# Kernel optimization log

Measured on AMD Instinct MI355X. Metric: run time of the kernel, lower is better.

## Reference

```python
import jax, jax.numpy as jnp
import numpy as np

FUZZYNUM = 4
EPS = 1e-5  # torch BatchNorm2d default


def conv2d(x, w, b):
    y = jax.lax.conv_general_dilated(x, w, (1, 1), 'SAME',
                                     dimension_numbers=('NCHW', 'OIHW', 'NCHW'))
    return y + b[None, :, None, None]


def batchnorm(x, gamma, beta):
    # training-mode BN: batch statistics over (N,H,W), biased variance
    m = jnp.mean(x, axis=(0, 2, 3), keepdims=True)
    v = jnp.mean((x - m) ** 2, axis=(0, 2, 3), keepdims=True)
    xn = (x - m) * jax.lax.rsqrt(v + EPS)
    return xn * gamma[None, :, None, None] + beta[None, :, None, None]


def fuzzify(x, lb_all, ub_all):
    # x: (N,1,H,W) -- conv1 output has 1 channel, so only bounds[0, f] are used.
    # Per-f sequential semantics of the original loop (x is mutated across f):
    #  in-range (ld>0 & ud>0): add exp(-0.5 ld^2)+exp(-0.5 ud^2)
    #  out-of-range (ld<0 or ud<0): reflect x -> 2*lb - x, then add
    #      exp(-0.5 ld^2) + exp(-0.5 (ub - x_new)^2)
    #  (the other sub-branches in the source are mathematically unreachable)
    fuzz = jnp.zeros_like(x)
    for f in range(FUZZYNUM):
        lb = lb_all[0, f]
        ub = ub_all[0, f]
        ld = x - lb
        ud = ub - x
        in_range = (ld > 0) & (ud > 0)
        out_range = (ld < 0) | (ud < 0)
        x_ref = 2.0 * lb - x
        c_in = jnp.exp(-0.5 * ld ** 2) + jnp.exp(-0.5 * ud ** 2)
        c_out = jnp.exp(-0.5 * ld ** 2) + jnp.exp(-0.5 * (ub - x_ref) ** 2)
        fuzz = fuzz + jnp.where(in_range, c_in, jnp.where(out_range, c_out, 0.0))
        x = jnp.where(out_range, x_ref, x)
    return fuzz


def setup_inputs() -> dict:
    key = jax.random.key(0)
    k0, k1, k2 = jax.random.split(key, 3)
    N, C, H, W = 16, 64, 256, 256
    sigma, init_mean = 2.0, 0.2
    x = jax.random.normal(k0, (N, C, H, W), dtype=jnp.float32)
    bnd1 = 1.0 / np.sqrt(C * 9)
    bnd2 = 1.0 / np.sqrt(1 * 9)
    conv1_w = jax.random.uniform(k1, (1, C, 3, 3), jnp.float32, -bnd1, bnd1)
    conv2_w = jax.random.uniform(k2, (C, 1, 3, 3), jnp.float32, -bnd2, bnd2)
    center = jnp.full((C, FUZZYNUM), init_mean, jnp.float32)
    return {
        'x': x,
        'conv1_w': conv1_w,
        'conv1_b': jnp.zeros((1,), jnp.float32),
        'conv2_w': conv2_w,
        'conv2_b': jnp.zeros((C,), jnp.float32),
        'bn1_g': jnp.ones((1,), jnp.float32),
        'bn1_b': jnp.zeros((1,), jnp.float32),
        'bn2_g': jnp.ones((C,), jnp.float32),
        'bn2_b': jnp.zeros((C,), jnp.float32),
        'lower_bound': center - sigma,
        'upper_bound': center + sigma,
    }


def reference(x, conv1_w, conv1_b, conv2_w, conv2_b, bn1_g, bn1_b, bn2_g, bn2_b,
              lower_bound, upper_bound):
    h = batchnorm(conv2d(x, conv1_w, conv1_b), bn1_g, bn1_b)  # (N,1,H,W)
    fz = fuzzify(h, lower_bound, upper_bound)                  # (N,1,H,W)
    return batchnorm(conv2d(fz, conv2_w, conv2_b), bn2_g, bn2_b)  # (N,C,H,W)
```

## Files before the change

### kernel.cpp

```cpp
#include <hip/hip_runtime.h>
#include <cstdint>

#define EPS 1e-5f
#define INV_NTOT (1.0f / 1048576.0f)

#define FZ_OFF  1048576
#define ST_OFF  2097152

__device__ __forceinline__ void dev_atomic_add(float* p, float v) {
    __hip_atomic_fetch_add(p, v, __ATOMIC_RELAXED, __HIP_MEMORY_SCOPE_AGENT);
}

__global__ __launch_bounds__(512) void k1_conv1(
    const float* __restrict__ x, const float* __restrict__ w1,
    float* __restrict__ h0, float* __restrict__ stats)
{
    __shared__ float tile[10][264];
    __shared__ float red_s[8], red_q[8];

    const int tid   = threadIdx.x;
    const int bid   = blockIdx.x;
    const int n     = bid >> 5;
    const int ht    = bid & 31;
    const int h0b   = ht << 3;

    const int t     = tid & 255;
    const int ohb   = (tid >> 8) << 2;
    const int rs    = tid >> 6;
    const int col4  = (tid & 63) << 2;

    float acc0 = 0.f, acc1 = 0.f, acc2 = 0.f, acc3 = 0.f;

    if (tid < 10) { tile[tid][3] = 0.f; tile[tid][260] = 0.f; }

    const float* xn = x + ((size_t)n << 22);

    for (int c = 0; c < 64; ++c) {
        __syncthreads();
        {
            int g = h0b - 1 + rs;
            float4 v = make_float4(0.f, 0.f, 0.f, 0.f);
            if ((unsigned)g < 256u)
                v = *(const float4*)(xn + ((size_t)c << 16) + (g << 8) + col4);
            *(float4*)&tile[rs][4 + col4] = v;
            if (rs < 2) {
                int g2 = h0b + 7 + rs;
                float4 v2 = make_float4(0.f, 0.f, 0.f, 0.f);
                if ((unsigned)g2 < 256u)
                    v2 = *(const float4*)(xn + ((size_t)c << 16) + (g2 << 8) + col4);
                *(float4*)&tile[8 + rs][4 + col4] = v2;
            }
        }
        __syncthreads();

        float wc[9];
        #pragma unroll
        for (int k = 0; k < 9; ++k) wc[k] = w1[c * 9 + k];

        #pragma unroll
        for (int rr = 0; rr < 6; ++rr) {
            const int sr = ohb + rr;
            float vm = tile[sr][3 + t];
            float v0 = tile[sr][4 + t];
            float vp = tile[sr][5 + t];
            #pragma unroll
            for (int di = 0; di < 3; ++di) {
                const int l = rr - di;
                if (l >= 0 && l < 4) {
                    float contrib = wc[di * 3 + 0] * vm + wc[di * 3 + 1] * v0
                                  + wc[di * 3 + 2] * vp;
                    if      (l == 0) acc0 += contrib;
                    else if (l == 1) acc1 += contrib;
                    else if (l == 2) acc2 += contrib;
                    else             acc3 += contrib;
                }
            }
        }
    }

    size_t ob = ((size_t)n << 16) + (size_t)((h0b + ohb) << 8) + t;
    h0[ob]       = acc0;
    h0[ob + 256] = acc1;
    h0[ob + 512] = acc2;
    h0[ob + 768] = acc3;

    float s  = acc0 + acc1 + acc2 + acc3;
    float sq = acc0 * acc0 + acc1 * acc1 + acc2 * acc2 + acc3 * acc3;
    #pragma unroll
    for (int o = 32; o > 0; o >>= 1) {
        s  += __shfl_down(s,  o, 64);
        sq += __shfl_down(sq, o, 64);
    }
    const int wave = tid >> 6, lane = tid & 63;
    if (lane == 0) { red_s[wave] = s; red_q[wave] = sq; }
    __syncthreads();
    if (tid == 0) {
        float S = 0.f, Q = 0.f;
        #pragma unroll
        for (int i = 0; i < 8; ++i) { S += red_s[i]; Q += red_q[i]; }
        dev_atomic_add(&stats[0], S);
        dev_atomic_add(&stats[1], Q);
    }
}

__global__ __launch_bounds__(256) void k3_fuzzify(
    const float* __restrict__ h0, const float* __restrict__ stats,
    const float* __restrict__ bn1_g, const float* __restrict__ bn1_b,
    const float* __restrict__ lb, const float* __restrict__ ub,
    float* __restrict__ fz)
{
    const int i = blockIdx.x * 256 + threadIdx.x;

    const float mean = stats[0] * INV_NTOT;
    const float var  = stats[1] * INV_NTOT - mean * mean;
    const float rstd = rsqrtf(var + EPS);
    const float A    = bn1_g[0] * rstd;
    const float B    = bn1_b[0] - mean * A;

    float lbv[4], ubv[4];
    #pragma unroll
    for (int f = 0; f < 4; ++f) { lbv[f] = lb[f]; ubv[f] = ub[f]; }

    float4 hv = *(const float4*)(h0 + (size_t)i * 4);
    float in[4] = { hv.x, hv.y, hv.z, hv.w };
    float res[4];
    #pragma unroll
    for (int k = 0; k < 4; ++k) {
        float xv = A * in[k] + B;
        float fuzz = 0.f;
        #pragma unroll
        for (int f = 0; f < 4; ++f) {
            float ld = xv - lbv[f];
            float ud = ubv[f] - xv;
            bool inr  = (ld > 0.f) && (ud > 0.f);
            bool outr = (ld < 0.f) || (ud < 0.f);
            float xr  = 2.f * lbv[f] - xv;
            float u2  = ubv[f] - xr;
            float e1  = __expf(-0.5f * ld * ld);
            float cin  = e1 + __expf(-0.5f * ud * ud);
            float cout = e1 + __expf(-0.5f * u2 * u2);
            fuzz += inr ? cin : (outr ? cout : 0.f);
            xv = outr ? xr : xv;
        }
        res[k] = fuzz;
    }
    *(float4*)(fz + (size_t)i * 4) = make_float4(res[0], res[1], res[2], res[3]);
}

__global__ __launch_bounds__(256) void k4_stats(
    const float* __restrict__ fz, float* __restrict__ stats)
{
    float s9[9], q45[45];
    #pragma unroll
    for (int i = 0; i < 9; ++i)  s9[i]  = 0.f;
    #pragma unroll
    for (int i = 0; i < 45; ++i) q45[i] = 0.f;

    const int base = blockIdx.x * 256 + threadIdx.x;
    for (int k = 0; k < 16; ++k) {
        int p = base + k * 65536;
        int w = p & 255, h = (p >> 8) & 255, n = p >> 16;
        const float* f = fz + ((size_t)n << 16);
        float v[9];
        #pragma unroll
        for (int di = 0; di < 3; ++di)
            #pragma unroll
            for (int dj = 0; dj < 3; ++dj) {
                int hh = h + di - 1, ww = w + dj - 1;
                v[di * 3 + dj] = ((unsigned)hh < 256u && (unsigned)ww < 256u)
                               ? f[(hh << 8) + ww] : 0.f;
            }
        int idx = 0;
        #pragma unroll
        for (int a = 0; a < 9; ++a) {
            s9[a] += v[a];
            #pragma unroll
            for (int b = a; b < 9; ++b) q45[idx++] += v[a] * v[b];
        }
    }

    __shared__ float red[4][54];
    const int wave = threadIdx.x >> 6, lane = threadIdx.x & 63;
    float vals[54];
    #pragma unroll
    for (int i = 0; i < 9; ++i)  vals[i]     = s9[i];
    #pragma unroll
    for (int i = 0; i < 45; ++i) vals[9 + i] = q45[i];
    #pragma unroll
    for (int i = 0; i < 54; ++i) {
        float vv = vals[i];
        #pragma unroll
        for (int o = 32; o > 0; o >>= 1) vv += __shfl_down(vv, o, 64);
        if (lane == 0) red[wave][i] = vv;
    }
    __syncthreads();
    if (threadIdx.x < 54) {
        float tot = red[0][threadIdx.x] + red[1][threadIdx.x]
                  + red[2][threadIdx.x] + red[3][threadIdx.x];
        dev_atomic_add(&stats[2 + threadIdx.x], tot);
    }
}

__global__ void k5_finalize(
    const float* __restrict__ w2, const float* __restrict__ bn2_g,
    const float* __restrict__ bn2_b, float* __restrict__ stats)
{
    const int c = threadIdx.x;
    if (c >= 64) return;
    float w[9];
    #pragma unroll
    for (int k = 0; k < 9; ++k) w[k] = w2[c * 9 + k];
    float P = 0.f;
    #pragma unroll
    for (int k = 0; k < 9; ++k) P += w[k] * stats[2 + k];
    P *= INV_NTOT;
    float QF = 0.f;
    int idx = 0;
    #pragma unroll
    for (int a = 0; a < 9; ++a)
        #pragma unroll
        for (int b = a; b < 9; ++b) {
            float qv = stats[11 + idx]; idx++;
            QF += w[a] * w[b] * qv * ((a == b) ? 1.f : 2.f);
        }
    QF *= INV_NTOT;
    float var   = QF - P * P;
    float scale = bn2_g[c] * rsqrtf(var + EPS);
    float bias  = bn2_b[c] - P * scale;
    stats[56 + c]  = scale;
    stats[120 + c] = bias;
}

__global__ __launch_bounds__(256) void k6_conv2(
    const float* __restrict__ fz, const float* __restrict__ w2,
    const float* __restrict__ stats, float* __restrict__ out)
{
    __shared__ float tile[34][36];
    const int bid = blockIdx.x;
    const int n   = bid >> 6;
    const int th  = (bid >> 3) & 7;
    const int tw  = bid & 7;
    const int h0b = th << 5, w0b = tw << 5;
    const int tid = threadIdx.x;

    const float* f = fz + ((size_t)n << 16);
    for (int i = tid; i < 34 * 34; i += 256) {
        int rr = i / 34, cc = i - rr * 34;
        int gh = h0b + rr - 1, gw = w0b + cc - 1;
        tile[rr][cc] = ((unsigned)gh < 256u && (unsigned)gw < 256u)
                     ? f[(gh << 8) + gw] : 0.f;
    }
    __syncthreads();

    const int r = tid >> 3, q = tid & 7;
    float v[3][6];
    #pragma unroll
    for (int di = 0; di < 3; ++di)
        #pragma unroll
        for (int j = 0; j < 6; ++j)
            v[di][j] = tile[r + di][(q << 2) + j];

    const size_t ob = ((size_t)n << 22) + (size_t)((h0b + r) << 8) + w0b + (q << 2);
    for (int c = 0; c < 64; ++c) {
        float wk[9];
        #pragma unroll
        for (int k = 0; k < 9; ++k) wk[k] = w2[c * 9 + k];
        const float sc = stats[56 + c], bi = stats[120 + c];
        float4 o;
        float* op = &o.x;
        #pragma unroll
        for (int k = 0; k < 4; ++k) {
            float y = 0.f;
            #pragma unroll
            for (int di = 0; di < 3; ++di)
                y += wk[di * 3 + 0] * v[di][k]
                   + wk[di * 3 + 1] * v[di][k + 1]
                   + wk[di * 3 + 2] * v[di][k + 2];
            op[k] = y * sc + bi;
        }
        *(float4*)(out + ob + ((size_t)c << 16)) = o;
    }
}

extern "C" void kernel_launch(void* const* d_in, const int* in_sizes, int n_in,
                              void* d_out, int out_size, void* d_ws, size_t ws_size,
                              hipStream_t stream)
{
    const float* x  = (const float*)d_in[0];
    const float* w1 = (const float*)d_in[1];
    const float* w2 = (const float*)d_in[3];
    const float* g1 = (const float*)d_in[5];
    const float* b1 = (const float*)d_in[6];
    const float* g2 = (const float*)d_in[7];
    const float* b2 = (const float*)d_in[8];
    const float* lb = (const float*)d_in[9];
    const float* ub = (const float*)d_in[10];

    float* ws  = (float*)d_ws;
    float* h0  = ws;
    float* fz  = ws + FZ_OFF;
    float* st  = ws + ST_OFF;
    float* out = (float*)d_out;

    hipMemsetAsync(st, 0, 56 * sizeof(float), stream);
    k1_conv1  <<<dim3(512),  dim3(512), 0, stream>>>(x, w1, h0, st);
    k3_fuzzify<<<dim3(1024), dim3(256), 0, stream>>>(h0, st, g1, b1, lb, ub, fz);
    k4_stats  <<<dim3(256),  dim3(256), 0, stream>>>(fz, st);
    k5_finalize<<<dim3(1),   dim3(64),  0, stream>>>(w2, g2, b2, st);
    k6_conv2  <<<dim3(1024), dim3(256), 0, stream>>>(fz, w2, st, out);
}
```

Baseline: 566.9 us.

## Fuse fuzzify with conv2 stats, fold BN2 finalize into conv2, remap conv1 blocks

Fuzzify is now computed into a shared-memory halo tile, and the 9/45 patch moment sums are accumulated from that tile in the same kernel. This removes the separate stats kernel and its strided global re-reads of fz. The single-block finalize kernel is dropped, and each conv2 block recomputes per-channel scale and bias into shared memory. Conv1 block indices are also permuted so neighbouring blocks land on different XCDs. The costs are halo recomputation of the exp-heavy fuzzify and redundant finalize work in every conv2 block.

```diff
diff --git a/kernel.cpp b/kernel.cpp
--- a/kernel.cpp
+++ b/kernel.cpp
@@ -19,9 +19,10 @@
     __shared__ float red_s[8], red_q[8];
 
     const int tid   = threadIdx.x;
-    const int bid   = blockIdx.x;
-    const int n     = bid >> 5;
-    const int ht    = bid & 31;
+    const int b     = blockIdx.x;
+    const int lin   = ((b & 7) << 6) + (b >> 3);
+    const int n     = lin >> 5;
+    const int ht    = lin & 31;
     const int h0b   = ht << 3;
 
     const int t     = tid & 255;
@@ -103,139 +104,15 @@
     }
 }
 
-__global__ __launch_bounds__(256) void k3_fuzzify(
-    const float* __restrict__ h0, const float* __restrict__ stats,
-    const float* __restrict__ bn1_g, const float* __restrict__ bn1_b,
-    const float* __restrict__ lb, const float* __restrict__ ub,
-    float* __restrict__ fz)
+__global__ __launch_bounds__(256) void k34_fuzzify_stats(
+    const float* __restrict__ h0, const float* __restrict__ bn1_g,
+    const float* __restrict__ bn1_b, const float* __restrict__ lb,
+    const float* __restrict__ ub, float* __restrict__ fz,
+    float* __restrict__ stats)
 {
-    const int i = blockIdx.x * 256 + threadIdx.x;
-
-    const float mean = stats[0] * INV_NTOT;
-    const float var  = stats[1] * INV_NTOT - mean * mean;
-    const float rstd = rsqrtf(var + EPS);
-    const float A    = bn1_g[0] * rstd;
-    const float B    = bn1_b[0] - mean * A;
-
-    float lbv[4], ubv[4];
-    #pragma unroll
-    for (int f = 0; f < 4; ++f) { lbv[f] = lb[f]; ubv[f] = ub[f]; }
-
-    float4 hv = *(const float4*)(h0 + (size_t)i * 4);
-    float in[4] = { hv.x, hv.y, hv.z, hv.w };
-    float res[4];
-    #pragma unroll
-    for (int k = 0; k < 4; ++k) {
-        float xv = A * in[k] + B;
-        float fuzz = 0.f;
-        #pragma unroll
-        for (int f = 0; f < 4; ++f) {
-            float ld = xv - lbv[f];
-            float ud = ubv[f] - xv;
-            bool inr  = (ld > 0.f) && (ud > 0.f);
-            bool outr = (ld < 0.f) || (ud < 0.f);
-            float xr  = 2.f * lbv[f] - xv;
-            float u2  = ubv[f] - xr;
-            float e1  = __expf(-0.5f * ld * ld);
-            float cin  = e1 + __expf(-0.5f * ud * ud);
-            float cout = e1 + __expf(-0.5f * u2 * u2);
-            fuzz += inr ? cin : (outr ? cout : 0.f);
-            xv = outr ? xr : xv;
-        }
-        res[k] = fuzz;
-    }
-    *(float4*)(fz + (size_t)i * 4) = make_float4(res[0], res[1], res[2], res[3]);
-}
-
-__global__ __launch_bounds__(256) void k4_stats(
-    const float* __restrict__ fz, float* __restrict__ stats)
-{
-    float s9[9], q45[45];
-    #pragma unroll
-    for (int i = 0; i < 9; ++i)  s9[i]  = 0.f;
-    #pragma unroll
-    for (int i = 0; i < 45; ++i) q45[i] = 0.f;
-
-    const int base = blockIdx.x * 256 + threadIdx.x;
-    for (int k = 0; k < 16; ++k) {
-        int p = base + k * 65536;
-        int w = p & 255, h = (p >> 8) & 255, n = p >> 16;
-        const float* f = fz + ((size_t)n << 16);
-        float v[9];
-        #pragma unroll
-        for (int di = 0; di < 3; ++di)
-            #pragma unroll
-            for (int dj = 0; dj < 3; ++dj) {
-                int hh = h + di - 1, ww = w + dj - 1;
-                v[di * 3 + dj] = ((unsigned)hh < 256u && (unsigned)ww < 256u)
-                               ? f[(hh << 8) + ww] : 0.f;
-            }
-        int idx = 0;
-        #pragma unroll
-        for (int a = 0; a < 9; ++a) {
-            s9[a] += v[a];
-            #pragma unroll
-            for (int b = a; b < 9; ++b) q45[idx++] += v[a] * v[b];
-        }
-    }
-
+    __shared__ float fzt[34][37];
     __shared__ float red[4][54];
-    const int wave = threadIdx.x >> 6, lane = threadIdx.x & 63;
-    float vals[54];
-    #pragma unroll
-    for (int i = 0; i < 9; ++i)  vals[i]     = s9[i];
-    #pragma unroll
-    for (int i = 0; i < 45; ++i) vals[9 + i] = q45[i];
-    #pragma unroll
-    for (int i = 0; i < 54; ++i) {
-        float vv = vals[i];
-        #pragma unroll
-        for (int o = 32; o > 0; o >>= 1) vv += __shfl_down(vv, o, 64);
-        if (lane == 0) red[wave][i] = vv;
-    }
-    __syncthreads();
-    if (threadIdx.x < 54) {
-        float tot = red[0][threadIdx.x] + red[1][threadIdx.x]
-                  + red[2][threadIdx.x] + red[3][threadIdx.x];
-        dev_atomic_add(&stats[2 + threadIdx.x], tot);
-    }
-}
-
-__global__ void k5_finalize(
-    const float* __restrict__ w2, const float* __restrict__ bn2_g,
-    const float* __restrict__ bn2_b, float* __restrict__ stats)
-{
-    const int c = threadIdx.x;
-    if (c >= 64) return;
-    float w[9];
-    #pragma unroll
-    for (int k = 0; k < 9; ++k) w[k] = w2[c * 9 + k];
-    float P = 0.f;
-    #pragma unroll
-    for (int k = 0; k < 9; ++k) P += w[k] * stats[2 + k];
-    P *= INV_NTOT;
-    float QF = 0.f;
-    int idx = 0;
-    #pragma unroll
-    for (int a = 0; a < 9; ++a)
-        #pragma unroll
-        for (int b = a; b < 9; ++b) {
-            float qv = stats[11 + idx]; idx++;
-            QF += w[a] * w[b] * qv * ((a == b) ? 1.f : 2.f);
-        }
-    QF *= INV_NTOT;
-    float var   = QF - P * P;
-    float scale = bn2_g[c] * rsqrtf(var + EPS);
-    float bias  = bn2_b[c] - P * scale;
-    stats[56 + c]  = scale;
-    stats[120 + c] = bias;
-}
-
-__global__ __launch_bounds__(256) void k6_conv2(
-    const float* __restrict__ fz, const float* __restrict__ w2,
-    const float* __restrict__ stats, float* __restrict__ out)
-{
-    __shared__ float tile[34][36];
+
     const int bid = blockIdx.x;
     const int n   = bid >> 6;
     const int th  = (bid >> 3) & 7;
@@ -243,6 +120,106 @@
     const int h0b = th << 5, w0b = tw << 5;
     const int tid = threadIdx.x;
 
+    const float mean = stats[0] * INV_NTOT;
+    const float var  = stats[1] * INV_NTOT - mean * mean;
+    const float rstd = rsqrtf(var + EPS);
+    const float A    = bn1_g[0] * rstd;
+    const float B    = bn1_b[0] - mean * A;
+
+    float lbv[4], ubv[4];
+    #pragma unroll
+    for (int f = 0; f < 4; ++f) { lbv[f] = lb[f]; ubv[f] = ub[f]; }
+
+    const float* hn = h0 + ((size_t)n << 16);
+    for (int i = tid; i < 34 * 34; i += 256) {
+        const int rr = i / 34, cc = i - rr * 34;
+        const int gh = h0b + rr - 1, gw = w0b + cc - 1;
+        float val = 0.f;
+        if ((unsigned)gh < 256u && (unsigned)gw < 256u) {
+            float xv = A * hn[(gh << 8) + gw] + B;
+            float fuzz = 0.f;
+            #pragma unroll
+            for (int f = 0; f < 4; ++f) {
+                float ld = xv - lbv[f];
+                float ud = ubv[f] - xv;
+                bool inr  = (ld > 0.f) && (ud > 0.f);
+                bool outr = (ld < 0.f) || (ud < 0.f);
+                float xr  = 2.f * lbv[f] - xv;
+                float u2  = ubv[f] - xr;
+                float e1  = __expf(-0.5f * ld * ld);
+                float cin  = e1 + __expf(-0.5f * ud * ud);
+                float cout = e1 + __expf(-0.5f * u2 * u2);
+                fuzz += inr ? cin : (outr ? cout : 0.f);
+                xv = outr ? xr : xv;
+            }
+            val = fuzz;
+        }
+        fzt[rr][cc] = val;
+    }
+    __syncthreads();
+
+    const int r = tid >> 3, q = (tid & 7) << 2;
+    float4 o = make_float4(fzt[r + 1][q + 1], fzt[r + 1][q + 2],
+                           fzt[r + 1][q + 3], fzt[r + 1][q + 4]);
+    *(float4*)(fz + ((size_t)n << 16) + (size_t)((h0b + r) << 8) + w0b + q) = o;
+
+    float s9[9], q45[45];
+    #pragma unroll
+    for (int i = 0; i < 9; ++i)  s9[i]  = 0.f;
+    #pragma unroll
+    for (int i = 0; i < 45; ++i) q45[i] = 0.f;
+
+    #pragma unroll
+    for (int k = 0; k < 4; ++k) {
+        float v[9];
+        #pragma unroll
+        for (int di = 0; di < 3; ++di)
+            #pragma unroll
+            for (int dj = 0; dj < 3; ++dj)
+                v[di * 3 + dj] = fzt[r + di][q + k + dj];
+        int idx = 0;
+        #pragma unroll
+        for (int a = 0; a < 9; ++a) {
+            s9[a] += v[a];
+            #pragma unroll
+            for (int bb = a; bb < 9; ++bb) q45[idx++] += v[a] * v[bb];
+        }
+    }
+
+    const int wave = tid >> 6, lane = tid & 63;
+    float vals[54];
+    #pragma unroll
+    for (int i = 0; i < 9; ++i)  vals[i]     = s9[i];
+    #pragma unroll
+    for (int i = 0; i < 45; ++i) vals[9 + i] = q45[i];
+    #pragma unroll
+    for (int i = 0; i < 54; ++i) {
+        float vv = vals[i];
+        #pragma unroll
+        for (int o2 = 32; o2 > 0; o2 >>= 1) vv += __shfl_down(vv, o2, 64);
+        if (lane == 0) red[wave][i] = vv;
+    }
+    __syncthreads();
+    if (tid < 54) {
+        float tot = red[0][tid] + red[1][tid] + red[2][tid] + red[3][tid];
+        dev_atomic_add(&stats[2 + tid], tot);
+    }
+}
+
+__global__ __launch_bounds__(256) void k6_conv2(
+    const float* __restrict__ fz, const float* __restrict__ w2,
+    const float* __restrict__ bn2_g, const float* __restrict__ bn2_b,
+    const float* __restrict__ stats, float* __restrict__ out)
+{
+    __shared__ float tile[34][37];
+    __shared__ float sc_s[64], bi_s[64];
+    const int bid = blockIdx.x;
+    const int n   = bid >> 6;
+    const int th  = (bid >> 3) & 7;
+    const int tw  = bid & 7;
+    const int h0b = th << 5, w0b = tw << 5;
+    const int tid = threadIdx.x;
+
     const float* f = fz + ((size_t)n << 16);
     for (int i = tid; i < 34 * 34; i += 256) {
         int rr = i / 34, cc = i - rr * 34;
@@ -250,6 +227,31 @@
         tile[rr][cc] = ((unsigned)gh < 256u && (unsigned)gw < 256u)
                      ? f[(gh << 8) + gw] : 0.f;
     }
+
+    if (tid < 64) {
+        const int c = tid;
+        float w[9];
+        #pragma unroll
+        for (int k = 0; k < 9; ++k) w[k] = w2[c * 9 + k];
+        float P = 0.f;
+        #pragma unroll
+        for (int k = 0; k < 9; ++k) P += w[k] * stats[2 + k];
+        P *= INV_NTOT;
+        float QF = 0.f;
+        int idx = 0;
+        #pragma unroll
+        for (int a = 0; a < 9; ++a)
+            #pragma unroll
+            for (int bb = a; bb < 9; ++bb) {
+                float qv = stats[11 + idx]; idx++;
+                QF += w[a] * w[bb] * qv * ((a == bb) ? 1.f : 2.f);
+            }
+        QF *= INV_NTOT;
+        float varc  = QF - P * P;
+        float scale = bn2_g[c] * rsqrtf(varc + EPS);
+        sc_s[c] = scale;
+        bi_s[c] = bn2_b[c] - P * scale;
+    }
     __syncthreads();
 
     const int r = tid >> 3, q = tid & 7;
@@ -265,7 +267,7 @@
         float wk[9];
         #pragma unroll
         for (int k = 0; k < 9; ++k) wk[k] = w2[c * 9 + k];
-        const float sc = stats[56 + c], bi = stats[120 + c];
+        const float sc = sc_s[c], bi = bi_s[c];
         float4 o;
         float* op = &o.x;
         #pragma unroll
@@ -303,9 +305,7 @@
     float* out = (float*)d_out;
 
     hipMemsetAsync(st, 0, 56 * sizeof(float), stream);
-    k1_conv1  <<<dim3(512),  dim3(512), 0, stream>>>(x, w1, h0, st);
-    k3_fuzzify<<<dim3(1024), dim3(256), 0, stream>>>(h0, st, g1, b1, lb, ub, fz);
-    k4_stats  <<<dim3(256),  dim3(256), 0, stream>>>(fz, st);
-    k5_finalize<<<dim3(1),   dim3(64),  0, stream>>>(w2, g2, b2, st);
-    k6_conv2  <<<dim3(1024), dim3(256), 0, stream>>>(fz, w2, st, out);
-}
+    k1_conv1         <<<dim3(512),  dim3(512), 0, stream>>>(x, w1, h0, st);
+    k34_fuzzify_stats<<<dim3(1024), dim3(256), 0, stream>>>(h0, g1, b1, lb, ub, fz, st);
+    k6_conv2         <<<dim3(1024), dim3(256), 0, stream>>>(fz, w2, g2, b2, st, out);
+}
```

Result: no change. 570.9 us (+0.7%).
